# Kernel tuning notes

Hardware: AMD Instinct MI355X
Metric: run time of the kernel (lower is better)

## Reference

```python
import jax, jax.numpy as jnp
import numpy as np

DIM = 2048
N_HEADS = 32
N_KV_HEADS = 8
HEAD_DIM = DIM // N_HEADS  # 64
GROUP = N_HEADS // N_KV_HEADS  # 4
ROPE_BASE = 10000.0


def setup_inputs() -> dict:
    key = jax.random.key(0)
    k1, k2, k3, k4, k5 = jax.random.split(key, 5)
    b, s = 1, 2048
    scale = 1.0 / np.sqrt(DIM)
    return {
        "x": jax.random.normal(k1, (b, s, DIM), dtype=jnp.float32),
        # weights stored as (in, out); equivalent math to torch Linear (x @ W.T)
        "wq": jax.random.normal(k2, (DIM, N_HEADS * HEAD_DIM), dtype=jnp.float32) * scale,
        "wk": jax.random.normal(k3, (DIM, N_KV_HEADS * HEAD_DIM), dtype=jnp.float32) * scale,
        "wv": jax.random.normal(k4, (DIM, N_KV_HEADS * HEAD_DIM), dtype=jnp.float32) * scale,
        "wo": jax.random.normal(k5, (N_HEADS * HEAD_DIM, DIM), dtype=jnp.float32) * scale,
    }


def _rope_cos_sin(seq_len, dtype):
    inv_freq = 1.0 / (ROPE_BASE ** (jnp.arange(0, HEAD_DIM, 2, dtype=jnp.float32) / HEAD_DIM))
    t = jnp.arange(seq_len, dtype=jnp.float32)
    freqs = jnp.outer(t, inv_freq)              # [s, hd/2]
    emb = jnp.concatenate([freqs, freqs], -1)   # [s, hd]
    return jnp.cos(emb).astype(dtype), jnp.sin(emb).astype(dtype)


def _rotate_half(x):
    x1, x2 = x[..., : HEAD_DIM // 2], x[..., HEAD_DIM // 2 :]
    return jnp.concatenate([-x2, x1], axis=-1)


def reference(x, wq, wk, wv, wo):
    b, s, _ = x.shape
    q = (x @ wq).reshape(b, s, N_HEADS, HEAD_DIM)
    k = (x @ wk).reshape(b, s, N_KV_HEADS, HEAD_DIM)
    v = (x @ wv).reshape(b, s, N_KV_HEADS, HEAD_DIM)

    cos, sin = _rope_cos_sin(s, x.dtype)
    cos = cos[None, :, None, :]  # [1, s, 1, hd] broadcast over batch & heads
    sin = sin[None, :, None, :]
    q = q * cos + _rotate_half(q) * sin
    k = k * cos + _rotate_half(k) * sin

    # GQA: repeat KV heads (repeat_interleave along head dim)
    k = jnp.repeat(k, GROUP, axis=2)  # [b, s, n_heads, hd]
    v = jnp.repeat(v, GROUP, axis=2)

    q = q.transpose(0, 2, 1, 3)  # [b, h, s, d]
    k = k.transpose(0, 2, 1, 3)
    v = v.transpose(0, 2, 1, 3)

    scores = jnp.einsum("bhqd,bhkd->bhqk", q, k) / jnp.sqrt(jnp.asarray(HEAD_DIM, x.dtype))
    attn = jax.nn.softmax(scores, axis=-1)
    out = jnp.einsum("bhqk,bhkd->bhqd", attn, v)
    out = out.transpose(0, 2, 1, 3).reshape(b, s, N_HEADS * HEAD_DIM)
    return out @ wo
```

## Files before the change

### kernel.cpp

```cpp
#include <hip/hip_runtime.h>
#include <hip/hip_bf16.h>

typedef __bf16 bf16x8 __attribute__((ext_vector_type(8)));
typedef __bf16 bf16x4 __attribute__((ext_vector_type(4)));
typedef __bf16 bf16x2 __attribute__((ext_vector_type(2)));
typedef float fx4 __attribute__((ext_vector_type(4)));
typedef float fx16 __attribute__((ext_vector_type(16)));

#define AS1 __attribute__((address_space(1)))
#define AS3 __attribute__((address_space(3)))

__global__ __launch_bounds__(256) void prep(const float4* __restrict__ X, __bf16* __restrict__ Xb,
                                            const float* __restrict__ wq, const float* __restrict__ wk,
                                            const float* __restrict__ wv, const float* __restrict__ wo,
                                            __bf16* __restrict__ WqkvT, __bf16* __restrict__ WoT) {
    const int bx = blockIdx.x;
    if (bx < 4096) {
        const int i = bx * 256 + threadIdx.x;
        const float4 v = X[i];
        bf16x4 o = { (__bf16)v.x, (__bf16)v.y, (__bf16)v.z, (__bf16)v.w };
        *(bf16x4*)(Xb + (size_t)i * 4) = o;
        return;
    }
    constexpr int K = 2048;
    __shared__ float t[64][33];
    const int tt = bx - 4096;
    const float* W; __bf16* Wt; int N, loc;
    if (tt < 2048)      { W = wq; Wt = WqkvT;                       N = 2048; loc = tt; }
    else if (tt < 2560) { W = wk; Wt = WqkvT + (size_t)2048 * 2048; N = 512;  loc = tt - 2048; }
    else if (tt < 3072) { W = wv; Wt = WqkvT + (size_t)2560 * 2048; N = 512;  loc = tt - 2560; }
    else                { W = wo; Wt = WoT;                         N = 2048; loc = tt - 3072; }
    const int k0 = (loc & 31) * 64, n0 = (loc >> 5) * 32;
    const int tx = threadIdx.x & 31, ty = threadIdx.x >> 5;
#pragma unroll
    for (int i = 0; i < 8; ++i)
        t[ty + i * 8][tx] = W[(size_t)(k0 + ty + i * 8) * N + n0 + tx];
    __syncthreads();
#pragma unroll
    for (int i = 0; i < 4; ++i) {
        const int nn = ty + i * 8;
        bf16x2 o = { (__bf16)t[tx * 2][nn], (__bf16)t[tx * 2 + 1][nn] };
        *(bf16x2*)&Wt[(size_t)(n0 + nn) * K + k0 + tx * 2] = o;
    }
}

__global__ __launch_bounds__(256) void gemm_qkv(const __bf16* __restrict__ A, const __bf16* __restrict__ Bt,
                                                __bf16* __restrict__ Qr, __bf16* __restrict__ Kr,
                                                __bf16* __restrict__ Vt) {
    constexpr int K = 2048;
    constexpr int BUF = 192 * 32;
    __shared__ __align__(16) __bf16 sm[2][BUF];
    const int tid = threadIdx.x;
    const int wave = tid >> 6, lane = tid & 63;
    const int quad = lane >> 4, l16 = lane & 15;
    const int m0 = blockIdx.x * 128, n0 = blockIdx.y * 64;
    fx4 acc[2][4] = {};

    const int r4 = lane >> 2;
    const int c8s = ((lane & 3) ^ ((r4 >> 1) & 3)) * 8;
    const __bf16* csrc[3]; int cdst[3];
#pragma unroll
    for (int it = 0; it < 3; ++it) {
        const int idx = wave * 3 + it;
        if (idx < 8) {
            csrc[it] = A + (size_t)(m0 + idx * 16 + r4) * K + c8s;
            cdst[it] = idx * 512 + lane * 8;
        } else {
            const int s = idx - 8;
            csrc[it] = Bt + (size_t)(n0 + s * 16 + r4) * K + c8s;
            cdst[it] = 4096 + s * 512 + lane * 8;
        }
    }
    const int colr = (quad ^ ((l16 >> 1) & 3)) * 8;
    const int arow = (wave * 32 + l16) * 32 + colr;
    const int brow = 4096 + l16 * 32 + colr;

#pragma unroll
    for (int it = 0; it < 3; ++it)
        __builtin_amdgcn_global_load_lds((const AS1 void*)csrc[it], (AS3 void*)&sm[0][cdst[it]], 16, 0, 0);
    __builtin_amdgcn_s_waitcnt(0);
    __syncthreads();

#pragma unroll 2
    for (int t = 0; t < 64; ++t) {
        if (t < 63) {
            const int kofs = (t + 1) * 32;
#pragma unroll
            for (int it = 0; it < 3; ++it)
                __builtin_amdgcn_global_load_lds((const AS1 void*)(csrc[it] + kofs),
                                                 (AS3 void*)&sm[(t + 1) & 1][cdst[it]], 16, 0, 0);
        }
        const __bf16* cb = sm[t & 1];
        bf16x8 af[2], bfr[4];
#pragma unroll
        for (int i = 0; i < 2; ++i) af[i] = *(const bf16x8*)&cb[arow + i * 512];
#pragma unroll
        for (int j = 0; j < 4; ++j) bfr[j] = *(const bf16x8*)&cb[brow + j * 512];
#pragma unroll
        for (int i = 0; i < 2; ++i)
#pragma unroll
            for (int j = 0; j < 4; ++j)
                acc[i][j] = __builtin_amdgcn_mfma_f32_16x16x32_bf16(af[i], bfr[j], acc[i][j], 0, 0, 0);
        if (t < 63) { __builtin_amdgcn_s_waitcnt(0); __syncthreads(); }
    }

    const int by = blockIdx.y;
    if (by < 40) {
        const float scale = (by < 32) ? 0.18033688011112042f : 1.0f;
        __bf16* base = (by < 32) ? (Qr + (size_t)by * 2048 * 64)
                                 : (Kr + (size_t)(by - 32) * 2048 * 64);
#pragma unroll
        for (int jj = 0; jj < 2; ++jj) {
            const int dlo = jj * 16 + l16;
            const float inv = __builtin_amdgcn_exp2f(-(float)dlo * 0.41524101186092029f);
#pragma unroll
            for (int i = 0; i < 2; ++i)
#pragma unroll
                for (int r = 0; r < 4; ++r) {
                    const int s = m0 + wave * 32 + i * 16 + quad * 4 + r;
                    float sn, cs;
                    __sincosf((float)s * inv, &sn, &cs);
                    const float lo = acc[i][jj][r], hv = acc[i][jj + 2][r];
                    base[(size_t)s * 64 + dlo]      = (__bf16)((lo * cs - hv * sn) * scale);
                    base[(size_t)s * 64 + dlo + 32] = (__bf16)((hv * cs + lo * sn) * scale);
                }
        }
    } else {
        __bf16* vb = Vt + (size_t)(by - 40) * 64 * 2048;
#pragma unroll
        for (int i = 0; i < 2; ++i)
#pragma unroll
            for (int j = 0; j < 4; ++j) {
                const int d = j * 16 + l16;
                const int s0 = m0 + wave * 32 + i * 16 + quad * 4;
                bf16x4 p;
#pragma unroll
                for (int r = 0; r < 4; ++r) p[r] = (__bf16)acc[i][j][r];
                *(bf16x4*)&vb[(size_t)d * 2048 + s0] = p;
            }
    }
}

__global__ __launch_bounds__(256) void gemm_bt_sk(const __bf16* __restrict__ A, const __bf16* __restrict__ Bt,
                                                  float* __restrict__ C0, float* __restrict__ C1,
                                                  int M, int N, int Kdim) {
    constexpr int K = 2048;
    constexpr int BUF = 256 * 32;
    __shared__ __align__(16) __bf16 sm[2][BUF];
    const int tid = threadIdx.x;
    const int wave = tid >> 6, lane = tid & 63;
    const int quad = lane >> 4, l16 = lane & 15;
    const int m0 = blockIdx.x * 128, n0 = blockIdx.y * 128;
    const int kz = blockIdx.z;
    float* C = kz ? C1 : C0;
    const int wm = (wave >> 1) * 64, wn = (wave & 1) * 64;
    fx4 acc[4][4] = {};

    const int r4 = lane >> 2;
    const int c8s = ((lane & 3) ^ ((r4 >> 1) & 3)) * 8;
    const __bf16* csrc[4]; int cdst[4];
#pragma unroll
    for (int it = 0; it < 4; ++it) {
        const int idx = wave * 4 + it;
        if (idx < 8) {
            csrc[it] = A + (size_t)(m0 + idx * 16 + r4) * K + c8s;
            cdst[it] = idx * 512 + lane * 8;
        } else {
            const int s = idx - 8;
            csrc[it] = Bt + (size_t)(n0 + s * 16 + r4) * K + c8s;
            cdst[it] = 4096 + s * 512 + lane * 8;
        }
    }
    const int colr = (quad ^ ((l16 >> 1) & 3)) * 8;
    const int arow = (wm + l16) * 32 + colr;
    const int brow = 4096 + (wn + l16) * 32 + colr;

    const int kbeg = kz * 1024;
#pragma unroll
    for (int it = 0; it < 4; ++it)
        __builtin_amdgcn_global_load_lds((const AS1 void*)(csrc[it] + kbeg), (AS3 void*)&sm[0][cdst[it]], 16, 0, 0);
    __builtin_amdgcn_s_waitcnt(0);
    __syncthreads();

#pragma unroll 2
    for (int t = 0; t < 32; ++t) {
        if (t < 31) {
            const int kofs = kbeg + (t + 1) * 32;
#pragma unroll
            for (int it = 0; it < 4; ++it)
                __builtin_amdgcn_global_load_lds((const AS1 void*)(csrc[it] + kofs),
                                                 (AS3 void*)&sm[(t + 1) & 1][cdst[it]], 16, 0, 0);
        }
        const __bf16* cb = sm[t & 1];
        bf16x8 af[4], bfr[4];
#pragma unroll
        for (int i = 0; i < 4; ++i) af[i] = *(const bf16x8*)&cb[arow + i * 512];
#pragma unroll
        for (int j = 0; j < 4; ++j) bfr[j] = *(const bf16x8*)&cb[brow + j * 512];
#pragma unroll
        for (int i = 0; i < 4; ++i)
#pragma unroll
            for (int j = 0; j < 4; ++j)
                acc[i][j] = __builtin_amdgcn_mfma_f32_16x16x32_bf16(af[i], bfr[j], acc[i][j], 0, 0, 0);
        if (t < 31) { __builtin_amdgcn_s_waitcnt(0); __syncthreads(); }
    }
#pragma unroll
    for (int i = 0; i < 4; ++i)
#pragma unroll
        for (int j = 0; j < 4; ++j) {
            const int row = m0 + wm + i * 16 + quad * 4;
            const int col = n0 + wn + j * 16 + l16;
#pragma unroll
            for (int r = 0; r < 4; ++r)
                C[(size_t)(row + r) * N + col] = acc[i][j][r];
        }
}

__global__ __launch_bounds__(256) void reduce_add(float4* __restrict__ out, const float4* __restrict__ p) {
    const int i = blockIdx.x * 256 + threadIdx.x;
    float4 a = out[i];
    const float4 b = p[i];
    a.x += b.x; a.y += b.y; a.z += b.z; a.w += b.w;
    out[i] = a;
}

__global__ __launch_bounds__(512, 4) void flash_attn(const __bf16* __restrict__ Qr, const __bf16* __restrict__ Kr,
                                                     const __bf16* __restrict__ Vt, __bf16* __restrict__ O) {
    constexpr int S = 2048;
    __shared__ __align__(16) __bf16 smem[2][4 * 64 * 72];
    const int qt = blockIdx.x, h = blockIdx.y, kvh = h >> 2;
    const int tid = threadIdx.x, wave = tid >> 6, lane = tid & 63;
    const int grp = wave >> 2, w4 = wave & 3;
    const int l32 = lane & 31, hi = lane >> 5;
    const int goff = grp * 2 * 4608;

    const int qrow = qt * 128 + w4 * 32 + l32;
    const __bf16* qptr = Qr + ((size_t)h * S + qrow) * 64;
    bf16x8 qf[4];
#pragma unroll
    for (int kc = 0; kc < 4; ++kc) qf[kc] = *(const bf16x8*)(qptr + kc * 16 + hi * 8);

    const __bf16* Kbase = Kr + (size_t)kvh * S * 64;
    const __bf16* Vbase = Vt + (size_t)kvh * 64 * S;

    const int gtid = tid & 255;
    const int krow = gtid >> 3;
    const int kcol = (gtid & 7) * 8;
    const int vslot = (kcol & 48) | ((kcol & 8) >> 1);

    bf16x8 kreg0 = *(const bf16x8*)(Kbase + (size_t)(grp * 64 + krow) * 64 + kcol);
    bf16x8 kreg1 = *(const bf16x8*)(Kbase + (size_t)(grp * 64 + 32 + krow) * 64 + kcol);
    bf16x8 vreg0 = *(const bf16x8*)(Vbase + (size_t)krow * S + grp * 64 + kcol);
    bf16x8 vreg1 = *(const bf16x8*)(Vbase + (size_t)(32 + krow) * S + grp * 64 + kcol);

    fx16 ov0, ov1;
#pragma unroll
    for (int i = 0; i < 16; ++i) { ov0[i] = 0.f; ov1[i] = 0.f; }
    float l_acc = 0.f;

    {
        __bf16* nK = &smem[0][goff];
        __bf16* nV = nK + 4608;
        *(bf16x8*)&nK[krow * 72 + kcol] = kreg0;
        *(bf16x8*)&nK[(32 + krow) * 72 + kcol] = kreg1;
        bf16x4 v0lo = { vreg0[0], vreg0[1], vreg0[2], vreg0[3] };
        bf16x4 v0hi = { vreg0[4], vreg0[5], vreg0[6], vreg0[7] };
        bf16x4 v1lo = { vreg1[0], vreg1[1], vreg1[2], vreg1[3] };
        bf16x4 v1hi = { vreg1[4], vreg1[5], vreg1[6], vreg1[7] };
        *(bf16x4*)&nV[krow * 72 + vslot]            = v0lo;
        *(bf16x4*)&nV[krow * 72 + vslot + 8]        = v0hi;
        *(bf16x4*)&nV[(32 + krow) * 72 + vslot]     = v1lo;
        *(bf16x4*)&nV[(32 + krow) * 72 + vslot + 8] = v1hi;
        const int kt1 = 2 + grp;
        kreg0 = *(const bf16x8*)(Kbase + (size_t)(kt1 * 64 + krow) * 64 + kcol);
        kreg1 = *(const bf16x8*)(Kbase + (size_t)(kt1 * 64 + 32 + krow) * 64 + kcol);
        vreg0 = *(const bf16x8*)(Vbase + (size_t)krow * S + kt1 * 64 + kcol);
        vreg1 = *(const bf16x8*)(Vbase + (size_t)(32 + krow) * S + kt1 * 64 + kcol);
    }
    __syncthreads();

    for (int it = 0; it < 16; ++it) {
        __bf16* lKg = &smem[it & 1][goff];
        __bf16* lVg = lKg + 4608;

        if (it + 1 < 16) {
            __bf16* nK = &smem[(it + 1) & 1][goff];
            __bf16* nV = nK + 4608;
            *(bf16x8*)&nK[krow * 72 + kcol] = kreg0;
            *(bf16x8*)&nK[(32 + krow) * 72 + kcol] = kreg1;
            bf16x4 v0lo = { vreg0[0], vreg0[1], vreg0[2], vreg0[3] };
            bf16x4 v0hi = { vreg0[4], vreg0[5], vreg0[6], vreg0[7] };
            bf16x4 v1lo = { vreg1[0], vreg1[1], vreg1[2], vreg1[3] };
            bf16x4 v1hi = { vreg1[4], vreg1[5], vreg1[6], vreg1[7] };
            *(bf16x4*)&nV[krow * 72 + vslot]            = v0lo;
            *(bf16x4*)&nV[krow * 72 + vslot + 8]        = v0hi;
            *(bf16x4*)&nV[(32 + krow) * 72 + vslot]     = v1lo;
            *(bf16x4*)&nV[(32 + krow) * 72 + vslot + 8] = v1hi;
            const int it2 = (it + 2 < 16) ? it + 2 : 15;
            const int ktn = it2 * 2 + grp;
            kreg0 = *(const bf16x8*)(Kbase + (size_t)(ktn * 64 + krow) * 64 + kcol);
            kreg1 = *(const bf16x8*)(Kbase + (size_t)(ktn * 64 + 32 + krow) * 64 + kcol);
            vreg0 = *(const bf16x8*)(Vbase + (size_t)krow * S + ktn * 64 + kcol);
            vreg1 = *(const bf16x8*)(Vbase + (size_t)(32 + krow) * S + ktn * 64 + kcol);
        }

        fx16 sc0, sc1;
#pragma unroll
        for (int i = 0; i < 16; ++i) { sc0[i] = 0.f; sc1[i] = 0.f; }
#pragma unroll
        for (int kc = 0; kc < 4; ++kc) {
            const bf16x8 a0 = *(const bf16x8*)&lKg[l32 * 72 + kc * 16 + hi * 8];
            const bf16x8 a1 = *(const bf16x8*)&lKg[(32 + l32) * 72 + kc * 16 + hi * 8];
            sc0 = __builtin_amdgcn_mfma_f32_32x32x16_bf16(a0, qf[kc], sc0, 0, 0, 0);
            sc1 = __builtin_amdgcn_mfma_f32_32x32x16_bf16(a1, qf[kc], sc1, 0, 0, 0);
        }

#pragma unroll
        for (int h2 = 0; h2 < 2; ++h2) {
#pragma unroll
            for (int c = 0; c < 2; ++c) {
                bf16x8 pb;
#pragma unroll
                for (int j = 0; j < 8; ++j) {
                    const float sv = h2 ? sc1[c * 8 + j] : sc0[c * 8 + j];
                    const float p = __builtin_amdgcn_exp2f(sv);
                    l_acc += p;
                    pb[j] = (__bf16)p;
                }
                const int kcv = h2 * 2 + c;
                const bf16x8 va0 = *(const bf16x8*)&lVg[l32 * 72 + kcv * 16 + hi * 8];
                const bf16x8 va1 = *(const bf16x8*)&lVg[(32 + l32) * 72 + kcv * 16 + hi * 8];
                ov0 = __builtin_amdgcn_mfma_f32_32x32x16_bf16(va0, pb, ov0, 0, 0, 0);
                ov1 = __builtin_amdgcn_mfma_f32_32x32x16_bf16(va1, pb, ov1, 0, 0, 0);
            }
        }
        __syncthreads();
    }

    const float l_pair = l_acc + __shfl_xor(l_acc, 32, 64);

    fx4* lO = (fx4*)&smem[0][0];
    float* lL = (float*)(&smem[0][0] + 16384);
    if (grp == 1) {
#pragma unroll
        for (int ic = 0; ic < 4; ++ic) {
            fx4 c0, c1;
#pragma unroll
            for (int r = 0; r < 4; ++r) { c0[r] = ov0[ic * 4 + r]; c1[r] = ov1[ic * 4 + r]; }
            lO[(ic * 4 + w4) * 64 + lane] = c0;
            lO[((ic + 4) * 4 + w4) * 64 + lane] = c1;
        }
        if (hi == 0) lL[w4 * 32 + l32] = l_pair;
    }
    __syncthreads();
    if (grp == 0) {
#pragma unroll
        for (int ic = 0; ic < 4; ++ic) {
            const fx4 c0 = lO[(ic * 4 + w4) * 64 + lane];
            const fx4 c1 = lO[((ic + 4) * 4 + w4) * 64 + lane];
#pragma unroll
            for (int r = 0; r < 4; ++r) { ov0[ic * 4 + r] += c0[r]; ov1[ic * 4 + r] += c1[r]; }
        }
        const float inv_l = 1.0f / (l_pair + lL[w4 * 32 + l32]);
#pragma unroll
        for (int dt = 0; dt < 2; ++dt)
#pragma unroll
            for (int rg2 = 0; rg2 < 4; ++rg2) {
                bf16x4 o4;
#pragma unroll
                for (int r = 0; r < 4; ++r)
                    o4[r] = (__bf16)((dt ? ov1[rg2 * 4 + r] : ov0[rg2 * 4 + r]) * inv_l);
                const int col = h * 64 + dt * 32 + rg2 * 8 + hi * 4;
                *(bf16x4*)(O + (size_t)qrow * 2048 + col) = o4;
            }
    }
}

extern "C" void kernel_launch(void* const* d_in, const int* in_sizes, int n_in,
                              void* d_out, int out_size, void* d_ws, size_t ws_size,
                              hipStream_t stream) {
    const float* x  = (const float*)d_in[0];
    const float* wq = (const float*)d_in[1];
    const float* wk = (const float*)d_in[2];
    const float* wv = (const float*)d_in[3];
    const float* wo = (const float*)d_in[4];
    float* out = (float*)d_out;
    char* ws = (char*)d_ws;

    __bf16* Xb    = (__bf16*)ws;
    __bf16* WqkvT = (__bf16*)(ws + ((size_t)8 << 20));
    __bf16* WoT   = (__bf16*)(ws + ((size_t)20 << 20));
    __bf16* Qr    = (__bf16*)(ws + ((size_t)28 << 20));
    __bf16* Kr    = (__bf16*)(ws + ((size_t)36 << 20));
    __bf16* Vt    = (__bf16*)(ws + ((size_t)38 << 20));
    __bf16* Ob    = (__bf16*)(ws + ((size_t)40 << 20));
    float*  Cp    = (float*)ws;

    prep<<<4096 + 5120, 256, 0, stream>>>((const float4*)x, Xb, wq, wk, wv, wo, WqkvT, WoT);
    gemm_qkv<<<dim3(16, 48), 256, 0, stream>>>(Xb, WqkvT, Qr, Kr, Vt);
    flash_attn<<<dim3(16, 32), 512, 0, stream>>>(Qr, Kr, Vt, Ob);
    gemm_bt_sk<<<dim3(16, 16, 2), 256, 0, stream>>>(Ob, WoT, out, Cp, 2048, 2048, 2048);
    reduce_add<<<4096, 256, 0, stream>>>((float4*)out, (const float4*)Cp);
}
```

Baseline: 214.6 us.

## Deepen GEMM pipelines to four LDS stages and drop split-K output projection

Both GEMMs now use a 4-deep LDS ring with three tiles in flight, partial vmcnt waits and a single barrier per k-step, replacing the double-buffer scheme that drained all loads every iteration. The output projection swaps its 128x128 split-K=2 kernel plus separate reduce_add pass for a 128x64 full-K kernel writing directly to the output. This removes the fp32 partial buffer round trip and one launch, at the cost of smaller tiles and more LDS per block.

Result: no change. 215.4 us (+0.4%).

```diff
diff --git a/kernel.cpp b/kernel.cpp
--- a/kernel.cpp
+++ b/kernel.cpp
@@ -49,7 +49,7 @@
                                                 __bf16* __restrict__ Vt) {
     constexpr int K = 2048;
     constexpr int BUF = 192 * 32;
-    __shared__ __align__(16) __bf16 sm[2][BUF];
+    __shared__ __align__(16) __bf16 sm[4][BUF];
     const int tid = threadIdx.x;
     const int wave = tid >> 6, lane = tid & 63;
     const int quad = lane >> 4, l16 = lane & 15;
@@ -75,22 +75,7 @@
     const int arow = (wave * 32 + l16) * 32 + colr;
     const int brow = 4096 + l16 * 32 + colr;
 
-#pragma unroll
-    for (int it = 0; it < 3; ++it)
-        __builtin_amdgcn_global_load_lds((const AS1 void*)csrc[it], (AS3 void*)&sm[0][cdst[it]], 16, 0, 0);
-    __builtin_amdgcn_s_waitcnt(0);
-    __syncthreads();
-
-#pragma unroll 2
-    for (int t = 0; t < 64; ++t) {
-        if (t < 63) {
-            const int kofs = (t + 1) * 32;
-#pragma unroll
-            for (int it = 0; it < 3; ++it)
-                __builtin_amdgcn_global_load_lds((const AS1 void*)(csrc[it] + kofs),
-                                                 (AS3 void*)&sm[(t + 1) & 1][cdst[it]], 16, 0, 0);
-        }
-        const __bf16* cb = sm[t & 1];
+    auto compute = [&](const __bf16* cb) {
         bf16x8 af[2], bfr[4];
 #pragma unroll
         for (int i = 0; i < 2; ++i) af[i] = *(const bf16x8*)&cb[arow + i * 512];
@@ -101,8 +86,29 @@
 #pragma unroll
             for (int j = 0; j < 4; ++j)
                 acc[i][j] = __builtin_amdgcn_mfma_f32_16x16x32_bf16(af[i], bfr[j], acc[i][j], 0, 0, 0);
-        if (t < 63) { __builtin_amdgcn_s_waitcnt(0); __syncthreads(); }
-    }
+    };
+
+#pragma unroll
+    for (int pt = 0; pt < 3; ++pt)
+#pragma unroll
+        for (int it = 0; it < 3; ++it)
+            __builtin_amdgcn_global_load_lds((const AS1 void*)(csrc[it] + pt * 32),
+                                             (AS3 void*)&sm[pt][cdst[it]], 16, 0, 0);
+
+#pragma unroll 1
+    for (int t = 0; t < 61; ++t) {
+        asm volatile("s_waitcnt vmcnt(6) lgkmcnt(0)" ::: "memory");
+        __builtin_amdgcn_s_barrier();
+        const int kofs = (t + 3) * 32;
+#pragma unroll
+        for (int it = 0; it < 3; ++it)
+            __builtin_amdgcn_global_load_lds((const AS1 void*)(csrc[it] + kofs),
+                                             (AS3 void*)&sm[(t + 3) & 3][cdst[it]], 16, 0, 0);
+        compute(sm[t & 3]);
+    }
+    asm volatile("s_waitcnt vmcnt(6) lgkmcnt(0)" ::: "memory"); __builtin_amdgcn_s_barrier(); compute(sm[1]);
+    asm volatile("s_waitcnt vmcnt(3) lgkmcnt(0)" ::: "memory"); __builtin_amdgcn_s_barrier(); compute(sm[2]);
+    asm volatile("s_waitcnt vmcnt(0) lgkmcnt(0)" ::: "memory"); __builtin_amdgcn_s_barrier(); compute(sm[3]);
 
     const int by = blockIdx.y;
     if (by < 40) {
@@ -141,27 +147,23 @@
     }
 }
 
-__global__ __launch_bounds__(256) void gemm_bt_sk(const __bf16* __restrict__ A, const __bf16* __restrict__ Bt,
-                                                  float* __restrict__ C0, float* __restrict__ C1,
-                                                  int M, int N, int Kdim) {
+__global__ __launch_bounds__(256) void gemm_out(const __bf16* __restrict__ A, const __bf16* __restrict__ Bt,
+                                                float* __restrict__ C) {
     constexpr int K = 2048;
-    constexpr int BUF = 256 * 32;
-    __shared__ __align__(16) __bf16 sm[2][BUF];
+    constexpr int BUF = 192 * 32;
+    __shared__ __align__(16) __bf16 sm[4][BUF];
     const int tid = threadIdx.x;
     const int wave = tid >> 6, lane = tid & 63;
     const int quad = lane >> 4, l16 = lane & 15;
-    const int m0 = blockIdx.x * 128, n0 = blockIdx.y * 128;
-    const int kz = blockIdx.z;
-    float* C = kz ? C1 : C0;
-    const int wm = (wave >> 1) * 64, wn = (wave & 1) * 64;
-    fx4 acc[4][4] = {};
+    const int m0 = blockIdx.x * 128, n0 = blockIdx.y * 64;
+    fx4 acc[2][4] = {};
 
     const int r4 = lane >> 2;
     const int c8s = ((lane & 3) ^ ((r4 >> 1) & 3)) * 8;
-    const __bf16* csrc[4]; int cdst[4];
-#pragma unroll
-    for (int it = 0; it < 4; ++it) {
-        const int idx = wave * 4 + it;
+    const __bf16* csrc[3]; int cdst[3];
+#pragma unroll
+    for (int it = 0; it < 3; ++it) {
+        const int idx = wave * 3 + it;
         if (idx < 8) {
             csrc[it] = A + (size_t)(m0 + idx * 16 + r4) * K + c8s;
             cdst[it] = idx * 512 + lane * 8;
@@ -172,56 +174,54 @@
         }
     }
     const int colr = (quad ^ ((l16 >> 1) & 3)) * 8;
-    const int arow = (wm + l16) * 32 + colr;
-    const int brow = 4096 + (wn + l16) * 32 + colr;
-
-    const int kbeg = kz * 1024;
-#pragma unroll
-    for (int it = 0; it < 4; ++it)
-        __builtin_amdgcn_global_load_lds((const AS1 void*)(csrc[it] + kbeg), (AS3 void*)&sm[0][cdst[it]], 16, 0, 0);
-    __builtin_amdgcn_s_waitcnt(0);
-    __syncthreads();
-
-#pragma unroll 2
-    for (int t = 0; t < 32; ++t) {
-        if (t < 31) {
-            const int kofs = kbeg + (t + 1) * 32;
-#pragma unroll
-            for (int it = 0; it < 4; ++it)
-                __builtin_amdgcn_global_load_lds((const AS1 void*)(csrc[it] + kofs),
-                                                 (AS3 void*)&sm[(t + 1) & 1][cdst[it]], 16, 0, 0);
-        }
-        const __bf16* cb = sm[t & 1];
-        bf16x8 af[4], bfr[4];
-#pragma unroll
-        for (int i = 0; i < 4; ++i) af[i] = *(const bf16x8*)&cb[arow + i * 512];
+    const int arow = (wave * 32 + l16) * 32 + colr;
+    const int brow = 4096 + l16 * 32 + colr;
+
+    auto compute = [&](const __bf16* cb) {
+        bf16x8 af[2], bfr[4];
+#pragma unroll
+        for (int i = 0; i < 2; ++i) af[i] = *(const bf16x8*)&cb[arow + i * 512];
 #pragma unroll
         for (int j = 0; j < 4; ++j) bfr[j] = *(const bf16x8*)&cb[brow + j * 512];
 #pragma unroll
-        for (int i = 0; i < 4; ++i)
+        for (int i = 0; i < 2; ++i)
 #pragma unroll
             for (int j = 0; j < 4; ++j)
                 acc[i][j] = __builtin_amdgcn_mfma_f32_16x16x32_bf16(af[i], bfr[j], acc[i][j], 0, 0, 0);
-        if (t < 31) { __builtin_amdgcn_s_waitcnt(0); __syncthreads(); }
-    }
-#pragma unroll
-    for (int i = 0; i < 4; ++i)
+    };
+
+#pragma unroll
+    for (int pt = 0; pt < 3; ++pt)
+#pragma unroll
+        for (int it = 0; it < 3; ++it)
+            __builtin_amdgcn_global_load_lds((const AS1 void*)(csrc[it] + pt * 32),
+                                             (AS3 void*)&sm[pt][cdst[it]], 16, 0, 0);
+
+#pragma unroll 1
+    for (int t = 0; t < 61; ++t) {
+        asm volatile("s_waitcnt vmcnt(6) lgkmcnt(0)" ::: "memory");
+        __builtin_amdgcn_s_barrier();
+        const int kofs = (t + 3) * 32;
+#pragma unroll
+        for (int it = 0; it < 3; ++it)
+            __builtin_amdgcn_global_load_lds((const AS1 void*)(csrc[it] + kofs),
+                                             (AS3 void*)&sm[(t + 3) & 3][cdst[it]], 16, 0, 0);
+        compute(sm[t & 3]);
+    }
+    asm volatile("s_waitcnt vmcnt(6) lgkmcnt(0)" ::: "memory"); __builtin_amdgcn_s_barrier(); compute(sm[1]);
+    asm volatile("s_waitcnt vmcnt(3) lgkmcnt(0)" ::: "memory"); __builtin_amdgcn_s_barrier(); compute(sm[2]);
+    asm volatile("s_waitcnt vmcnt(0) lgkmcnt(0)" ::: "memory"); __builtin_amdgcn_s_barrier(); compute(sm[3]);
+
+#pragma unroll
+    for (int i = 0; i < 2; ++i)
 #pragma unroll
         for (int j = 0; j < 4; ++j) {
-            const int row = m0 + wm + i * 16 + quad * 4;
-            const int col = n0 + wn + j * 16 + l16;
+            const int row = m0 + wave * 32 + i * 16 + quad * 4;
+            const int col = n0 + j * 16 + l16;
 #pragma unroll
             for (int r = 0; r < 4; ++r)
-                C[(size_t)(row + r) * N + col] = acc[i][j][r];
-        }
-}
-
-__global__ __launch_bounds__(256) void reduce_add(float4* __restrict__ out, const float4* __restrict__ p) {
-    const int i = blockIdx.x * 256 + threadIdx.x;
-    float4 a = out[i];
-    const float4 b = p[i];
-    a.x += b.x; a.y += b.y; a.z += b.z; a.w += b.w;
-    out[i] = a;
+                C[(size_t)(row + r) * 2048 + col] = acc[i][j][r];
+        }
 }
 
 __global__ __launch_bounds__(512, 4) void flash_attn(const __bf16* __restrict__ Qr, const __bf16* __restrict__ Kr,
@@ -394,11 +394,9 @@
     __bf16* Kr    = (__bf16*)(ws + ((size_t)36 << 20));
     __bf16* Vt    = (__bf16*)(ws + ((size_t)38 << 20));
     __bf16* Ob    = (__bf16*)(ws + ((size_t)40 << 20));
-    float*  Cp    = (float*)ws;
 
     prep<<<4096 + 5120, 256, 0, stream>>>((const float4*)x, Xb, wq, wk, wv, wo, WqkvT, WoT);
     gemm_qkv<<<dim3(16, 48), 256, 0, stream>>>(Xb, WqkvT, Qr, Kr, Vt);
     flash_attn<<<dim3(16, 32), 512, 0, stream>>>(Qr, Kr, Vt, Ob);
-    gemm_bt_sk<<<dim3(16, 16, 2), 256, 0, stream>>>(Ob, WoT, out, Cp, 2048, 2048, 2048);
-    reduce_add<<<4096, 256, 0, stream>>>((float4*)out, (const float4*)Cp);
+    gemm_out<<<dim3(16, 32), 256, 0, stream>>>(Ob, WoT, out);
 }
```
